# Optimization experiments

Hardware: AMD Instinct MI355X
Metric: run time of the kernel (lower is better)

## Reference

```python
import jax, jax.numpy as jnp
import numpy as np

A = 9          # num anchors (RPN.anchor_list)
H = W = 32     # feature-map spatial size (scaled-up from 7x7)
HID = 256      # ProposalModule hidden dim
THRESH = 0.5       # inference() thresh default
NMS_THRESH = 0.7   # inference() nms_thresh default
N = H * W * A


def _conv(x, w, b):
    y = jax.lax.conv_general_dilated(x, w, (1, 1), 'SAME',
                                     dimension_numbers=('NCHW', 'OIHW', 'NCHW'))
    return y + b[None, :, None, None]


def _pairwise_iou(boxes):
    # boxes: (N,4) [x1,y1,x2,y2]
    x1, y1, x2, y2 = boxes[:, 0], boxes[:, 1], boxes[:, 2], boxes[:, 3]
    area = jnp.maximum(x2 - x1, 0.) * jnp.maximum(y2 - y1, 0.)
    iw = jnp.maximum(jnp.minimum(x2[:, None], x2[None, :]) - jnp.maximum(x1[:, None], x1[None, :]), 0.)
    ih = jnp.maximum(jnp.minimum(y2[:, None], y2[None, :]) - jnp.maximum(y1[:, None], y1[None, :]), 0.)
    inter = iw * ih
    return inter / (area[:, None] + area[None, :] - inter + 1e-8)


def _nms_keep(boxes, scores, valid, iou_thresh):
    # greedy NMS over ALL boxes; invalid (below conf-thresh) boxes start suppressed
    n = boxes.shape[0]
    order = jnp.argsort(-scores)
    b = boxes[order]
    v = valid[order]
    iou = _pairwise_iou(b)            # (N,N) -- dominant memory traffic
    idx = jnp.arange(n)

    def body(i, sup):
        alive = jnp.logical_not(sup[i])
        return sup | (alive & (iou[i] > iou_thresh) & (idx > i))

    sup = jax.lax.fori_loop(0, n, body, jnp.logical_not(v))
    return jnp.zeros(n, bool).at[order].set(jnp.logical_not(sup))


def setup_inputs() -> dict:
    key = jax.random.key(0)
    ks = jax.random.split(key, 4)
    feat = jax.random.normal(ks[0], (1, 1280, H, W), jnp.float32)
    anchors_wh = jnp.array([[1, 1], [2, 2], [3, 3], [4, 4], [5, 5],
                            [2, 3], [3, 2], [3, 5], [5, 3]], jnp.float32)
    w1 = jax.random.normal(ks[1], (HID, 1280, 3, 3), jnp.float32) * 0.01
    b1 = jnp.zeros((HID,), jnp.float32)
    w2 = jax.random.normal(ks[2], (6 * A, HID, 1, 1), jnp.float32) * 0.05
    b2 = jax.random.normal(ks[3], (6 * A,), jnp.float32) * 0.05
    return {"feat": feat, "anchors_wh": anchors_wh, "w1": w1, "b1": b1, "w2": w2, "b2": b2}


def reference(feat, anchors_wh, w1, b1, w2, b2):
    # ProposalModule: 3x3 conv + LeakyReLU + 1x1 conv to 6A channels (dropout is identity at inference)
    h = jax.nn.leaky_relu(_conv(feat, w1, b1), 0.01)
    out = _conv(h, w2, b2)[0].reshape(A, 6, H, W)   # batch 1 -> (A,6,H,W)
    conf = jax.nn.sigmoid(out[:, 0])                 # (A,H,W), sigmoid(conf_scores[:,0])
    offs = out[:, 2:6].transpose(0, 2, 3, 1)         # (A,H,W,4) = offsets.permute(0,2,3,1)

    # GenerateGrid: cell centers at +0.5; GenerateAnchor: wh-sized boxes on each center
    xs = jnp.arange(W, dtype=feat.dtype) + 0.5
    ys = jnp.arange(H, dtype=feat.dtype) + 0.5
    cx = xs[None, None, :]
    cy = ys[None, :, None]
    aw = anchors_wh[:, 0][:, None, None]
    ah = anchors_wh[:, 1][:, None, None]

    tx, ty, tw, th = offs[..., 0], offs[..., 1], offs[..., 2], offs[..., 3]
    pcx = cx + tx * aw
    pcy = cy + ty * ah
    pw = aw * jnp.exp(tw)
    ph = ah * jnp.exp(th)
    boxes = jnp.stack([pcx - pw / 2, pcy - ph / 2, pcx + pw / 2, pcy + ph / 2], -1)  # (A,H,W,4)

    conf_f = conf.transpose(1, 2, 0).reshape(-1)          # (H*W*A,) = permute(1,2,0).reshape(-1)
    boxes_f = boxes.transpose(1, 2, 0, 3).reshape(-1, 4)  # (H*W*A,4)

    valid = conf_f > THRESH
    scores = jnp.where(valid, conf_f, -1.0)
    keep = _nms_keep(boxes_f, scores, valid, NMS_THRESH)

    k = keep.astype(boxes_f.dtype)[:, None]
    # fixed-shape masked output: kept rows are [x1,y1,x2,y2,conf], suppressed rows are 0
    return jnp.concatenate([boxes_f * k, conf_f[:, None] * k], axis=-1)  # (N,5)
```

## Files before the change

### kernel.cpp

```cpp
#include <hip/hip_runtime.h>
#include <math.h>

#define NPIX 1024
#define NBOX 9216
#define ECAP 6144

typedef unsigned long long u64;

#define O_PART     0u
#define O_H        0u
#define O_BOXES    1048576u
#define O_CONF     1196032u
#define O_KEYS     1232896u
#define O_ORDER    1306624u
#define O_SBOX     1343488u
#define O_SAREA    1490944u
#define O_EDGES    1527808u
#define O_KEEPW    1552384u
#define O_RPART    1553920u
#define O_VCNT     16777216u
#define O_ECNT     16777220u


#define GLOAD_LDS16(g, l)                                            \
    __builtin_amdgcn_global_load_lds(                                \
        (const __attribute__((address_space(1))) void*)(g),          \
        (__attribute__((address_space(3))) void*)(l), 16, 0, 0)

__global__ __launch_bounds__(256, 4) void conv1_kernel(const float* __restrict__ feat,
                                                       const float* __restrict__ w1,
                                                       float* __restrict__ partial,
                                                       int* __restrict__ VE) {
    const int kc  = blockIdx.x;
    const int cog = blockIdx.y;
    const int tid = threadIdx.x;
    const int x0 = (tid & 7) * 4;
    const int y  = tid >> 3;
    const int ci0 = kc * 80;
    const int co0 = cog * 4;

    if (kc == 0 && cog == 0 && tid < 2) VE[tid] = 0;

    __shared__ float sf[8 * 34 * 32];

    for (int e = tid; e < 8 * 2 * 32; e += 256) {
        int ci_l = e >> 6, r = (e >> 5) & 1, c = e & 31;
        sf[(ci_l * 34 + r * 33) * 32 + c] = 0.f;
    }

    float acc[4][4];
#pragma unroll
    for (int a = 0; a < 4; ++a)
#pragma unroll
        for (int b = 0; b < 4; ++b) acc[a][b] = 0.f;

    const float* wbase = w1 + (size_t)co0 * 11520 + (size_t)ci0 * 9;
    const int wid = tid >> 6, lane = tid & 63;

    for (int chunk = 0; chunk < 10; ++chunk) {
        const int cbase = ci0 + chunk * 8;
        __syncthreads();
        {
            const float4* fg = (const float4*)(feat + (size_t)cbase * NPIX);
#pragma unroll
            for (int k = 0; k < 8; ++k)
                GLOAD_LDS16(fg + k * 256 + tid,
                            &sf[(k * 34 + 1) * 32 + wid * 256 + lane * 4]);
        }
        __syncthreads();

#pragma unroll
        for (int cil = 0; cil < 8; ++cil) {
            float f[3][6];
            const float* base = &sf[(cil * 34 + y) * 32];
#pragma unroll
            for (int dy = 0; dy < 3; ++dy) {
                const float* rp = base + dy * 32;
                float4 mid = *(const float4*)(rp + x0);
                float lft = __int_as_float(__builtin_amdgcn_update_dpp(
                    0, __float_as_int(mid.w), 0x111 , 0xF, 0xF, true));
                float rgt = __int_as_float(__builtin_amdgcn_update_dpp(
                    0, __float_as_int(mid.x), 0x101 , 0xF, 0xF, true));
                f[dy][0] = (x0 == 0) ? 0.f : lft;
                f[dy][1] = mid.x; f[dy][2] = mid.y; f[dy][3] = mid.z; f[dy][4] = mid.w;
                f[dy][5] = (x0 == 28) ? 0.f : rgt;
            }
#pragma unroll
            for (int co = 0; co < 4; ++co) {
                const float* wrow = wbase + (size_t)co * 11520 +
                                    (size_t)(chunk * 8 + cil) * 9;
                float wv[9];
#pragma unroll
                for (int t = 0; t < 9; ++t) wv[t] = wrow[t];
#pragma unroll
                for (int dy = 0; dy < 3; ++dy)
#pragma unroll
                    for (int dx = 0; dx < 3; ++dx) {
                        float wgt = wv[dy * 3 + dx];
#pragma unroll
                        for (int px = 0; px < 4; ++px)
                            acc[co][px] = fmaf(f[dy][px + dx], wgt, acc[co][px]);
                    }
            }
        }
    }

    const int pix = y * 32 + x0;
#pragma unroll
    for (int co = 0; co < 4; ++co) {
        float4 v = {acc[co][0], acc[co][1], acc[co][2], acc[co][3]};
        *(float4*)&partial[((size_t)kc * 256 + co0 + co) * NPIX + pix] = v;
    }
}

__global__ __launch_bounds__(256) void conv1_reduce(float* part_h,
                                                    const float* __restrict__ b1) {
    int i = blockIdx.x * 256 + threadIdx.x;
    float s = b1[i >> 10];
#pragma unroll
    for (int kc = 0; kc < 16; ++kc) s += part_h[(size_t)kc * 262144 + i];
    part_h[i] = s > 0.f ? s : 0.01f * s;
}

__global__ __launch_bounds__(256) void conv2_decode(const float* __restrict__ h,
                                                    const float* __restrict__ w2,
                                                    const float* __restrict__ b2,
                                                    const float* __restrict__ anchors,
                                                    float* __restrict__ boxes,
                                                    float* __restrict__ conf_arr,
                                                    u64* __restrict__ keys,
                                                    int* __restrict__ Vcnt) {
    int gid = blockIdx.x * 256 + threadIdx.x;
    int box = gid >> 2, q = gid & 3;
    int a = box >> 10, p = box & 1023;
    const float* hq  = h + (size_t)(q * 64) * NPIX + p;
    const float* wb  = w2 + (size_t)(a * 6) * 256 + q * 64;
    float s0 = 0.f, s2 = 0.f, s3 = 0.f, s4 = 0.f, s5 = 0.f;
#pragma unroll 4
    for (int ci = 0; ci < 64; ++ci) {
        float hv = hq[(size_t)ci * NPIX];
        s0 = fmaf(hv, wb[0 * 256 + ci], s0);
        s2 = fmaf(hv, wb[2 * 256 + ci], s2);
        s3 = fmaf(hv, wb[3 * 256 + ci], s3);
        s4 = fmaf(hv, wb[4 * 256 + ci], s4);
        s5 = fmaf(hv, wb[5 * 256 + ci], s5);
    }
    s0 += __shfl_xor(s0, 1); s0 += __shfl_xor(s0, 2);
    s2 += __shfl_xor(s2, 1); s2 += __shfl_xor(s2, 2);
    s3 += __shfl_xor(s3, 1); s3 += __shfl_xor(s3, 2);
    s4 += __shfl_xor(s4, 1); s4 += __shfl_xor(s4, 2);
    s5 += __shfl_xor(s5, 1); s5 += __shfl_xor(s5, 2);
    if (q == 0) {
        s0 += b2[a * 6 + 0];
        s2 += b2[a * 6 + 2];
        s3 += b2[a * 6 + 3];
        s4 += b2[a * 6 + 4];
        s5 += b2[a * 6 + 5];
        float conf = 1.f / (1.f + expf(-s0));
        float x = (float)(p & 31), yy = (float)(p >> 5);
        float cx = x + 0.5f, cy = yy + 0.5f;
        float aw = anchors[a * 2 + 0], ah = anchors[a * 2 + 1];
        float pcx = cx + s2 * aw, pcy = cy + s3 * ah;
        float pw = aw * expf(s4), ph = ah * expf(s5);
        int idx = p * 9 + a;
        boxes[idx * 4 + 0] = pcx - pw / 2.f;
        boxes[idx * 4 + 1] = pcy - ph / 2.f;
        boxes[idx * 4 + 2] = pcx + pw / 2.f;
        boxes[idx * 4 + 3] = pcy + ph / 2.f;
        conf_arr[idx] = conf;
        bool valid = conf > 0.5f;
        float score = valid ? conf : -1.0f;
        unsigned int sb = __float_as_uint(score);
        sb = (sb & 0x80000000u) ? ~sb : (sb | 0x80000000u);
        keys[idx] = ((u64)sb << 32) | (unsigned int)(~idx);
        if (valid) atomicAdd(Vcnt, 1);
    }
}

__global__ __launch_bounds__(256) void rank_partial(const u64* __restrict__ keys,
                                                    int* __restrict__ rpart) {
    __shared__ u64 sk[256];
    int i = blockIdx.x * 256 + threadIdx.x;
    sk[threadIdx.x] = keys[blockIdx.y * 256 + threadIdx.x];
    __syncthreads();
    u64 ki = keys[i];
    int c = 0;
#pragma unroll 8
    for (int j = 0; j < 256; ++j) c += (sk[j] > ki) ? 1 : 0;
    rpart[blockIdx.y * NBOX + i] = c;
}

__global__ __launch_bounds__(256) void rank_reduce_gather(const int* __restrict__ rpart,
                                                          const float* __restrict__ boxes,
                                                          int* __restrict__ order,
                                                          float* __restrict__ sbox,
                                                          float* __restrict__ sarea) {
    int i = blockIdx.x * 256 + threadIdx.x;
    int r = 0;
    for (int b = 0; b < 36; ++b) r += rpart[b * NBOX + i];
    order[r] = i;
    float x1 = boxes[i * 4 + 0], y1 = boxes[i * 4 + 1];
    float x2 = boxes[i * 4 + 2], y2 = boxes[i * 4 + 3];
    sbox[r * 4 + 0] = x1; sbox[r * 4 + 1] = y1;
    sbox[r * 4 + 2] = x2; sbox[r * 4 + 3] = y2;
    sarea[r] = fmaxf(x2 - x1, 0.f) * fmaxf(y2 - y1, 0.f);
}

__global__ __launch_bounds__(256) void nms_edges(const float* __restrict__ sbox,
                                                 const float* __restrict__ sarea,
                                                 const int* __restrict__ Vp,
                                                 unsigned* __restrict__ edges,
                                                 int* __restrict__ Ecnt) {
    int i = blockIdx.x;
    int V = *Vp;
    if (i >= V) return;
    float x1i = sbox[i * 4 + 0], y1i = sbox[i * 4 + 1];
    float x2i = sbox[i * 4 + 2], y2i = sbox[i * 4 + 3];
    float ai = sarea[i];
    int lane = threadIdx.x & 63;
    for (int j = i + 1 + threadIdx.x; ; j += 256) {
        bool active = (j < V);
        if (__ballot(active) == 0ull) break;
        bool hit = false;
        if (active) {
            float x1j = sbox[j * 4 + 0], y1j = sbox[j * 4 + 1];
            float x2j = sbox[j * 4 + 2], y2j = sbox[j * 4 + 3];
            float iw = fmaxf(fminf(x2i, x2j) - fmaxf(x1i, x1j), 0.f);
            float ih = fmaxf(fminf(y2i, y2j) - fmaxf(y1i, y1j), 0.f);
            float inter = iw * ih;
            float iou = inter / (ai + sarea[j] - inter + 1e-8f);
            hit = iou > 0.7f;
        }
        u64 bal = __ballot(hit);
        if (bal) {
            int cnt = __popcll(bal);
            unsigned base = 0;
            if (lane == 0) base = (unsigned)atomicAdd(Ecnt, cnt);
            base = (unsigned)__shfl((int)base, 0, 64);
            if (hit) {
                int pos = (int)base + __popcll(bal & ((1ull << lane) - 1ull));
                if (pos < ECAP) edges[pos] = ((unsigned)j << 16) | (unsigned)i;
            }
        }
    }
}

__global__ __launch_bounds__(256) void nms_resolve_finalize(const unsigned* __restrict__ edges,
                                                            const int* __restrict__ Ep,
                                                            const int* __restrict__ Vp,
                                                            const int* __restrict__ order,
                                                            const float* __restrict__ boxes,
                                                            const float* __restrict__ conf_arr,
                                                            float* __restrict__ out) {
    __shared__ unsigned se[ECAP];
    __shared__ unsigned ss[ECAP];
    __shared__ u64 sup[144];
    const int tid = threadIdx.x;
    int E = *Ep; if (E > ECAP) E = ECAP;
    const int V = *Vp;
    for (int e = tid; e < E; e += 256) se[e] = edges[e];
    for (int w = tid; w < 144; w += 256) sup[w] = 0;
    __syncthreads();
    for (int e = tid; e < E; e += 256) {
        unsigned k = se[e];
        int r = 0;
        for (int q = 0; q < E; ++q) r += (se[q] < k) ? 1 : 0;
        ss[r] = k;
    }
    __syncthreads();
    if (tid == 0) {
        for (int e = 0; e < E; ++e) {
            unsigned k = ss[e];
            int i = (int)(k & 0xffffu), j = (int)(k >> 16);
            if (!((sup[i >> 6] >> (i & 63)) & 1ull))
                sup[j >> 6] |= 1ull << (j & 63);
        }
    }
    __syncthreads();
    for (int p = tid; p < NBOX; p += 256) {
        int o = order[p];
        bool keep = (p < V) && !((sup[p >> 6] >> (p & 63)) & 1ull);
        float k = keep ? 1.f : 0.f;
        out[o * 5 + 0] = boxes[o * 4 + 0] * k;
        out[o * 5 + 1] = boxes[o * 4 + 1] * k;
        out[o * 5 + 2] = boxes[o * 4 + 2] * k;
        out[o * 5 + 3] = boxes[o * 4 + 3] * k;
        out[o * 5 + 4] = conf_arr[o] * k;
    }
}

extern "C" void kernel_launch(void* const* d_in, const int* in_sizes, int n_in,
                              void* d_out, int out_size, void* d_ws, size_t ws_size,
                              hipStream_t stream) {
    const float* feat    = (const float*)d_in[0];
    const float* anchors = (const float*)d_in[1];
    const float* w1      = (const float*)d_in[2];
    const float* b1      = (const float*)d_in[3];
    const float* w2      = (const float*)d_in[4];
    const float* b2      = (const float*)d_in[5];
    float* out = (float*)d_out;

    char* ws = (char*)d_ws;
    float* partial = (float*)(ws + O_PART);
    float* h       = (float*)(ws + O_H);
    float* boxes   = (float*)(ws + O_BOXES);
    float* conf    = (float*)(ws + O_CONF);
    u64*   keys    = (u64*)(ws + O_KEYS);
    int* rpart     = (int*)(ws + O_RPART);
    int* order     = (int*)(ws + O_ORDER);
    float* sbox    = (float*)(ws + O_SBOX);
    float* sarea   = (float*)(ws + O_SAREA);
    int* Vcnt      = (int*)(ws + O_VCNT);
    int* Ecnt      = (int*)(ws + O_ECNT);
    unsigned* edges = (unsigned*)(ws + O_EDGES);

    conv1_kernel<<<dim3(16, 64), 256, 0, stream>>>(feat, w1, partial, Vcnt);
    conv1_reduce<<<1024, 256, 0, stream>>>(partial, b1);
    conv2_decode<<<144, 256, 0, stream>>>(h, w2, b2, anchors, boxes, conf, keys, Vcnt);
    rank_partial<<<dim3(36, 36), 256, 0, stream>>>(keys, rpart);
    rank_reduce_gather<<<36, 256, 0, stream>>>(rpart, boxes, order, sbox, sarea);
    nms_edges<<<NBOX, 256, 0, stream>>>(sbox, sarea, Vcnt, edges, Ecnt);
    nms_resolve_finalize<<<1, 256, 0, stream>>>(edges, Ecnt, Vcnt, order, boxes, conf, out);
}
```

Measured before the change: 248.1 us.

## Fuse conv1 reduction into conv2 decode and merge rank kernels

```diff
diff --git a/kernel.cpp b/kernel.cpp
--- a/kernel.cpp
+++ b/kernel.cpp
@@ -8,24 +8,16 @@
 typedef unsigned long long u64;
 
 #define O_PART     0u
-#define O_H        0u
-#define O_BOXES    1048576u
-#define O_CONF     1196032u
-#define O_KEYS     1232896u
-#define O_ORDER    1306624u
-#define O_SBOX     1343488u
-#define O_SAREA    1490944u
-#define O_EDGES    1527808u
-#define O_KEEPW    1552384u
-#define O_RPART    1553920u
 #define O_VCNT     16777216u
 #define O_ECNT     16777220u
-
-
-#define GLOAD_LDS16(g, l)                                            \
-    __builtin_amdgcn_global_load_lds(                                \
-        (const __attribute__((address_space(1))) void*)(g),          \
-        (__attribute__((address_space(3))) void*)(l), 16, 0, 0)
+#define O_BOXES    16777224u
+#define O_CONF     16924680u
+#define O_KEYS     16961544u
+#define O_ORDER    17035272u
+#define O_SBOX     17072136u
+#define O_SAREA    17219592u
+#define O_EDGES    17256456u
+
 
 __global__ __launch_bounds__(256, 4) void conv1_kernel(const float* __restrict__ feat,
                                                        const float* __restrict__ w1,
@@ -55,7 +47,6 @@
         for (int b = 0; b < 4; ++b) acc[a][b] = 0.f;
 
     const float* wbase = w1 + (size_t)co0 * 11520 + (size_t)ci0 * 9;
-    const int wid = tid >> 6, lane = tid & 63;
 
     for (int chunk = 0; chunk < 10; ++chunk) {
         const int cbase = ci0 + chunk * 8;
@@ -63,9 +54,13 @@
         {
             const float4* fg = (const float4*)(feat + (size_t)cbase * NPIX);
 #pragma unroll
-            for (int k = 0; k < 8; ++k)
-                GLOAD_LDS16(fg + k * 256 + tid,
-                            &sf[(k * 34 + 1) * 32 + wid * 256 + lane * 4]);
+            for (int k = 0; k < 8; ++k) {
+                int e = tid + k * 256;
+                int ci_l = e >> 8, rem = e & 255;
+                int row = rem >> 3, f4c = rem & 7;
+                float4 v = fg[ci_l * 256 + rem];
+                *(float4*)&sf[(ci_l * 34 + row + 1) * 32 + f4c * 4] = v;
+            }
         }
         __syncthreads();
 
@@ -113,16 +108,8 @@
     }
 }
 
-__global__ __launch_bounds__(256) void conv1_reduce(float* part_h,
-                                                    const float* __restrict__ b1) {
-    int i = blockIdx.x * 256 + threadIdx.x;
-    float s = b1[i >> 10];
-#pragma unroll
-    for (int kc = 0; kc < 16; ++kc) s += part_h[(size_t)kc * 262144 + i];
-    part_h[i] = s > 0.f ? s : 0.01f * s;
-}
-
-__global__ __launch_bounds__(256) void conv2_decode(const float* __restrict__ h,
+__global__ __launch_bounds__(256) void conv2_decode(const float* __restrict__ partial,
+                                                    const float* __restrict__ b1,
                                                     const float* __restrict__ w2,
                                                     const float* __restrict__ b2,
                                                     const float* __restrict__ anchors,
@@ -131,25 +118,30 @@
                                                     u64* __restrict__ keys,
                                                     int* __restrict__ Vcnt) {
     int gid = blockIdx.x * 256 + threadIdx.x;
-    int box = gid >> 2, q = gid & 3;
+    int box = gid >> 3, q = gid & 7;
     int a = box >> 10, p = box & 1023;
-    const float* hq  = h + (size_t)(q * 64) * NPIX + p;
-    const float* wb  = w2 + (size_t)(a * 6) * 256 + q * 64;
+    const float* pbase = partial + (size_t)(q * 32) * NPIX + p;
+    const float* wq    = w2 + (size_t)(a * 6) * 256 + q * 32;
+    const float* b1q   = b1 + q * 32;
     float s0 = 0.f, s2 = 0.f, s3 = 0.f, s4 = 0.f, s5 = 0.f;
 #pragma unroll 4
-    for (int ci = 0; ci < 64; ++ci) {
-        float hv = hq[(size_t)ci * NPIX];
-        s0 = fmaf(hv, wb[0 * 256 + ci], s0);
-        s2 = fmaf(hv, wb[2 * 256 + ci], s2);
-        s3 = fmaf(hv, wb[3 * 256 + ci], s3);
-        s4 = fmaf(hv, wb[4 * 256 + ci], s4);
-        s5 = fmaf(hv, wb[5 * 256 + ci], s5);
-    }
-    s0 += __shfl_xor(s0, 1); s0 += __shfl_xor(s0, 2);
-    s2 += __shfl_xor(s2, 1); s2 += __shfl_xor(s2, 2);
-    s3 += __shfl_xor(s3, 1); s3 += __shfl_xor(s3, 2);
-    s4 += __shfl_xor(s4, 1); s4 += __shfl_xor(s4, 2);
-    s5 += __shfl_xor(s5, 1); s5 += __shfl_xor(s5, 2);
+    for (int ci = 0; ci < 32; ++ci) {
+        float hv = b1q[ci];
+#pragma unroll
+        for (int kc = 0; kc < 16; ++kc)
+            hv += pbase[(size_t)kc * 262144 + (size_t)ci * NPIX];
+        hv = hv > 0.f ? hv : 0.01f * hv;
+        s0 = fmaf(hv, wq[0 * 256 + ci], s0);
+        s2 = fmaf(hv, wq[2 * 256 + ci], s2);
+        s3 = fmaf(hv, wq[3 * 256 + ci], s3);
+        s4 = fmaf(hv, wq[4 * 256 + ci], s4);
+        s5 = fmaf(hv, wq[5 * 256 + ci], s5);
+    }
+    s0 += __shfl_xor(s0, 1); s0 += __shfl_xor(s0, 2); s0 += __shfl_xor(s0, 4);
+    s2 += __shfl_xor(s2, 1); s2 += __shfl_xor(s2, 2); s2 += __shfl_xor(s2, 4);
+    s3 += __shfl_xor(s3, 1); s3 += __shfl_xor(s3, 2); s3 += __shfl_xor(s3, 4);
+    s4 += __shfl_xor(s4, 1); s4 += __shfl_xor(s4, 2); s4 += __shfl_xor(s4, 4);
+    s5 += __shfl_xor(s5, 1); s5 += __shfl_xor(s5, 2); s5 += __shfl_xor(s5, 4);
     if (q == 0) {
         s0 += b2[a * 6 + 0];
         s2 += b2[a * 6 + 2];
@@ -177,33 +169,38 @@
     }
 }
 
-__global__ __launch_bounds__(256) void rank_partial(const u64* __restrict__ keys,
-                                                    int* __restrict__ rpart) {
-    __shared__ u64 sk[256];
-    int i = blockIdx.x * 256 + threadIdx.x;
-    sk[threadIdx.x] = keys[blockIdx.y * 256 + threadIdx.x];
+__global__ __launch_bounds__(1024) void rank_gather(const u64* __restrict__ keys,
+                                                    const float* __restrict__ boxes,
+                                                    int* __restrict__ order,
+                                                    float* __restrict__ sbox,
+                                                    float* __restrict__ sarea) {
+    __shared__ u64 sk[4][256];
+    __shared__ int pr[4][256];
+    const int tid = threadIdx.x;
+    const int qr = tid >> 8, li = tid & 255;
+    const int i = blockIdx.x * 256 + li;
+    const u64 ki = keys[i];
+    int c = 0;
+    for (int t = 0; t < 9; ++t) {
+        int tile = qr + t * 4;
+        sk[qr][li] = keys[tile * 256 + li];
+        __syncthreads();
+        const u64* s = sk[qr];
+#pragma unroll 8
+        for (int j = 0; j < 256; ++j) c += (s[j] > ki) ? 1 : 0;
+        __syncthreads();
+    }
+    pr[qr][li] = c;
     __syncthreads();
-    u64 ki = keys[i];
-    int c = 0;
-#pragma unroll 8
-    for (int j = 0; j < 256; ++j) c += (sk[j] > ki) ? 1 : 0;
-    rpart[blockIdx.y * NBOX + i] = c;
-}
-
-__global__ __launch_bounds__(256) void rank_reduce_gather(const int* __restrict__ rpart,
-                                                          const float* __restrict__ boxes,
-                                                          int* __restrict__ order,
-                                                          float* __restrict__ sbox,
-                                                          float* __restrict__ sarea) {
-    int i = blockIdx.x * 256 + threadIdx.x;
-    int r = 0;
-    for (int b = 0; b < 36; ++b) r += rpart[b * NBOX + i];
-    order[r] = i;
-    float x1 = boxes[i * 4 + 0], y1 = boxes[i * 4 + 1];
-    float x2 = boxes[i * 4 + 2], y2 = boxes[i * 4 + 3];
-    sbox[r * 4 + 0] = x1; sbox[r * 4 + 1] = y1;
-    sbox[r * 4 + 2] = x2; sbox[r * 4 + 3] = y2;
-    sarea[r] = fmaxf(x2 - x1, 0.f) * fmaxf(y2 - y1, 0.f);
+    if (qr == 0) {
+        int r = pr[0][li] + pr[1][li] + pr[2][li] + pr[3][li];
+        order[r] = i;
+        float x1 = boxes[i * 4 + 0], y1 = boxes[i * 4 + 1];
+        float x2 = boxes[i * 4 + 2], y2 = boxes[i * 4 + 3];
+        sbox[r * 4 + 0] = x1; sbox[r * 4 + 1] = y1;
+        sbox[r * 4 + 2] = x2; sbox[r * 4 + 3] = y2;
+        sarea[r] = fmaxf(x2 - x1, 0.f) * fmaxf(y2 - y1, 0.f);
+    }
 }
 
 __global__ __launch_bounds__(256) void nms_edges(const float* __restrict__ sbox,
@@ -302,11 +299,9 @@
 
     char* ws = (char*)d_ws;
     float* partial = (float*)(ws + O_PART);
-    float* h       = (float*)(ws + O_H);
     float* boxes   = (float*)(ws + O_BOXES);
     float* conf    = (float*)(ws + O_CONF);
     u64*   keys    = (u64*)(ws + O_KEYS);
-    int* rpart     = (int*)(ws + O_RPART);
     int* order     = (int*)(ws + O_ORDER);
     float* sbox    = (float*)(ws + O_SBOX);
     float* sarea   = (float*)(ws + O_SAREA);
@@ -315,10 +310,9 @@
     unsigned* edges = (unsigned*)(ws + O_EDGES);
 
     conv1_kernel<<<dim3(16, 64), 256, 0, stream>>>(feat, w1, partial, Vcnt);
-    conv1_reduce<<<1024, 256, 0, stream>>>(partial, b1);
-    conv2_decode<<<144, 256, 0, stream>>>(h, w2, b2, anchors, boxes, conf, keys, Vcnt);
-    rank_partial<<<dim3(36, 36), 256, 0, stream>>>(keys, rpart);
-    rank_reduce_gather<<<36, 256, 0, stream>>>(rpart, boxes, order, sbox, sarea);
+    conv2_decode<<<288, 256, 0, stream>>>(partial, b1, w2, b2, anchors,
+                                          boxes, conf, keys, Vcnt);
+    rank_gather<<<36, 1024, 0, stream>>>(keys, boxes, order, sbox, sarea);
     nms_edges<<<NBOX, 256, 0, stream>>>(sbox, sarea, Vcnt, edges, Ecnt);
     nms_resolve_finalize<<<1, 256, 0, stream>>>(edges, Ecnt, Vcnt, order, boxes, conf, out);
 }
```

New measurement: 331.3 us. 1.34x slower.
